# Optimization experiments

Hardware: AMD Instinct MI355X
Metric: run time of the kernel (lower is better)

The kernel has to match this reference:

```python
import jax, jax.numpy as jnp
import numpy as np

B, R, N, K, E = 128, 500, 500, 10, 128
H1 = 5 * E  # UnvisitedMLP hidden = embedding_dim * 5


def setup_inputs() -> dict:
    key = jax.random.key(0)
    ks = jax.random.split(key, 8)
    current = jax.random.randint(ks[0], (B, R), 0, N)
    distance = jax.random.uniform(ks[1], (B, N, N), dtype=jnp.float32)
    # unvisited cities, exercising the padding-index path in search_unvisited.
    visited = jax.random.uniform(ks[2], (B, R, N)) < 0.97
    masked = jnp.where(visited, -jnp.inf, 0.0).astype(jnp.float32)
    encoded_nodes = jax.random.normal(ks[3], (B, N, E), dtype=jnp.float32)
    w1 = jax.random.normal(ks[4], (H1, K * E), dtype=jnp.float32) * (1.0 / np.sqrt(K * E))
    b1 = jnp.zeros((H1,), dtype=jnp.float32)
    w2 = jax.random.normal(ks[5], (E, H1), dtype=jnp.float32) * (1.0 / np.sqrt(H1))
    b2 = jnp.zeros((E,), dtype=jnp.float32)
    return {"current": current, "distance": distance, "masked": masked,
            "encoded_nodes": encoded_nodes, "w1": w1, "b1": b1, "w2": w2, "b2": b2}


def _search_unvisited(current, distance, masked, k_near):
    # distance_filtered[b, r, :] = distance[b, current[b, r], :]  -> [B, R, N]
    b_idx = jnp.arange(current.shape[0])[:, None]
    distance_filtered = distance[b_idx, current, :]
    mask_unvisited = masked != -jnp.inf
    distance_masked = jnp.where(mask_unvisited, distance_filtered, jnp.inf)
    # k smallest == top-k of negated distances
    neg_vals, k_idx = jax.lax.top_k(-distance_masked, k_near)  # [B, R, K]
    is_inf = neg_vals == -jnp.inf  # entries that were +inf (no unvisited left)
    n_cities = distance.shape[1]
    return jnp.where(is_inf, n_cities, k_idx)  # padding index = problem_size


def _gather_pad0(encoded_nodes, idx):
    # pad encoded_nodes with a zero row at index N, then gather  -> [B, R, K, E]
    padded = jnp.concatenate(
        [encoded_nodes, jnp.zeros_like(encoded_nodes[:, :1, :])], axis=1)
    b_idx = jnp.arange(encoded_nodes.shape[0])[:, None, None]
    return padded[b_idx, idx, :]


def _pad_avg(a):
    # replace all-zero (padding) rows along K with the mean of non-zero rows
    is_zero = a.sum(axis=-1) == 0  # [B, R, K]
    nz_count = jnp.clip((~is_zero).sum(axis=-1).astype(jnp.float32), 1e-9)
    mean_vec = a.sum(axis=2) / nz_count[..., None]  # [B, R, E]
    return jnp.where(is_zero[..., None], mean_vec[:, :, None, :], a)


def reference(current, distance, masked, encoded_nodes, w1, b1, w2, b2):
    k_near = K
    idx = _search_unvisited(current, distance, masked, k_near)  # [B, R, K]
    emb = _gather_pad0(encoded_nodes, idx)                      # [B, R, K, E]
    emb = _pad_avg(emb)
    h = emb.reshape(emb.shape[0], emb.shape[1], k_near * emb.shape[-1])  # [B, R, K*E]
    h = jax.nn.relu(jnp.einsum('brf,hf->brh', h, w1) + b1)
    out = jnp.einsum('brh,eh->bre', h, w2) + b2  # [B, R, E]
    return out
```

## Files before the change

kernel.cpp:

```cpp
#include <hip/hip_runtime.h>
#include <cstdint>
#include <cstddef>

#define Bn   128
#define Rn   500
#define Nn   500
#define Kn   10
#define En   128
#define H1n  640
#define KEn  1280
#define Mn   (Bn * Rn)

typedef short s16x8 __attribute__((ext_vector_type(8)));
typedef float f32x4 __attribute__((ext_vector_type(4)));

__device__ __forceinline__ unsigned short f2bf(float x) {
    union { float f; unsigned int u; } v; v.f = x;
    unsigned int r = v.u + 0x7fffu + ((v.u >> 16) & 1u);
    return (unsigned short)(r >> 16);
}
__device__ __forceinline__ float bf2f(unsigned short u) {
    union { unsigned int u; float f; } v; v.u = ((unsigned int)u) << 16;
    return v.f;
}
__device__ __forceinline__ void gl2lds16(const void* g, void* l) {
    __builtin_amdgcn_global_load_lds(
        (const __attribute__((address_space(1))) unsigned int*)g,
        (__attribute__((address_space(3))) unsigned int*)l, 16, 0, 0);
}
__device__ __forceinline__ void drain_all() {
    asm volatile("s_waitcnt vmcnt(0) lgkmcnt(0)" ::: "memory");
}

__global__ void convw_kernel(const float* __restrict__ enc, const float* __restrict__ w1,
                             const float* __restrict__ w2,
                             unsigned short* __restrict__ encb, unsigned short* __restrict__ w1b,
                             unsigned short* __restrict__ w2b) {
    int i = blockIdx.x * 256 + threadIdx.x;
    if (i < (Bn * Nn * En) / 4) {
        float4 v = ((const float4*)enc)[i];
        ushort4 o; o.x = f2bf(v.x); o.y = f2bf(v.y); o.z = f2bf(v.z); o.w = f2bf(v.w);
        ((ushort4*)encb)[i] = o;
    }
    if (i < (H1n * KEn) / 4) {
        float4 v = ((const float4*)w1)[i];
        ushort4 o; o.x = f2bf(v.x); o.y = f2bf(v.y); o.z = f2bf(v.z); o.w = f2bf(v.w);
        ((ushort4*)w1b)[i] = o;
    }
    if (i < (En * H1n) / 4) {
        float4 v = ((const float4*)w2)[i];
        ushort4 o; o.x = f2bf(v.x); o.y = f2bf(v.y); o.z = f2bf(v.z); o.w = f2bf(v.w);
        ((ushort4*)w2b)[i] = o;
    }
}

__global__ __launch_bounds__(256) void select_kernel(const int* __restrict__ current,
                            const float* __restrict__ distance,
                            const float* __restrict__ masked,
                            const unsigned short* __restrict__ encb,
                            int* __restrict__ idx_out,
                            unsigned short* __restrict__ meanbb) {
    const int row  = blockIdx.x * 4 + (threadIdx.x >> 6);
    const int lane = threadIdx.x & 63;
    const int b    = row / Rn;
    const int cur  = current[row];
    const unsigned int* drow = (const unsigned int*)(distance + ((size_t)b * Nn + cur) * Nn);
    const unsigned int* mrow = (const unsigned int*)(masked + (size_t)row * Nn);

    unsigned long long key[8];
#pragma unroll
    for (int i = 0; i < 8; ++i) {
        int nn = lane + 64 * i;
        unsigned int fb = 0x7F800000u;
        if (nn < Nn) {
            unsigned int m = mrow[nn];
            unsigned int d = drow[nn];
            fb = (m == 0xFF800000u) ? 0x7F800000u : d;
        }
        key[i] = ((unsigned long long)fb << 32) | (unsigned int)nn;
    }

    int ids[Kn];
    int myid = Nn;
#pragma unroll
    for (int it = 0; it < Kn; ++it) {
        unsigned long long bk = key[0];
#pragma unroll
        for (int i = 1; i < 8; ++i) bk = (key[i] < bk) ? key[i] : bk;
#pragma unroll
        for (int off = 1; off < 64; off <<= 1) {
            unsigned long long ok = __shfl_xor(bk, off);
            bk = (ok < bk) ? ok : bk;
        }
        const int wid = ((bk >> 32) == 0x7F800000u) ? Nn : (int)(bk & 0xffffffffu);
        ids[it] = wid;
        if (lane == it) myid = wid;
#pragma unroll
        for (int i = 0; i < 8; ++i)
            if (key[i] == bk) key[i] = 0x7F800000FFFFFFFFull;
    }
    if (lane < Kn) idx_out[row * Kn + lane] = myid;

    const unsigned int* encu = (const unsigned int*)(encb + (size_t)b * Nn * En);
    float s0 = 0.f, s1 = 0.f; int cnt = 0;
#pragma unroll
    for (int k = 0; k < Kn; ++k) {
        const int id = ids[k];
        if (id < Nn) {
            unsigned int u = encu[id * (En / 2) + lane];
            s0 += bf2f((unsigned short)(u & 0xffffu));
            s1 += bf2f((unsigned short)(u >> 16));
            cnt++;
        }
    }
    float m0 = 0.f, m1 = 0.f;
    if (cnt > 0) { m0 = s0 / (float)cnt; m1 = s1 / (float)cnt; }
    unsigned int packed = (unsigned int)f2bf(m0) | ((unsigned int)f2bf(m1) << 16);
    ((unsigned int*)meanbb)[(size_t)row * (En / 2) + lane] = packed;
}

__global__ __launch_bounds__(256, 4) void gemm1_kernel(
        const unsigned short* __restrict__ encb, const unsigned short* __restrict__ meanbb,
        const int* __restrict__ idxb, const unsigned short* __restrict__ w1b,
        const float* __restrict__ b1, unsigned short* __restrict__ hbuf) {
    __shared__ alignas(16) unsigned short As[2][128 * 32];
    __shared__ alignas(16) unsigned short Bs[2][128 * 32];
    __shared__ int idxs[128 * Kn];

    const int p = blockIdx.x;
    const int L = (p & 7) * 313 + (p >> 3);
    if (L >= (Mn / 128) * (H1n / 128)) return;
    const int row0 = (L / 5) * 128;
    const int h0   = (L % 5) * 128;

    const int t    = threadIdx.x;
    const int lane = t & 63;
    const int wave = t >> 6;
    const int ln15 = lane & 15;
    const int q4   = lane >> 4;
    const int wm   = wave & 1;
    const int wn   = wave >> 1;

    for (int i = t; i < 128 * Kn; i += 256) idxs[i] = idxb[row0 * Kn + i];

    const int rl   = lane >> 2;
    const int sc   = lane & 3;
    const int coff = (sc ^ (rl & 3)) * 8;

    int lrow[2];
    const unsigned short* encB[2];
    const unsigned short* meanR[2];
    const unsigned short* w1R[2];
#pragma unroll
    for (int s = 0; s < 2; ++s) {
        lrow[s] = wave * 32 + s * 16 + rl;
        const int gr = row0 + lrow[s];
        const int bb = gr / Rn;
        encB[s]  = encb + (size_t)bb * Nn * En;
        meanR[s] = meanbb + (size_t)gr * En + coff;
        w1R[s]   = w1b + (size_t)(h0 + lrow[s]) * KEn + coff;
    }

    f32x4 acc[4][4];
#pragma unroll
    for (int i = 0; i < 4; ++i)
#pragma unroll
        for (int j = 0; j < 4; ++j)
            acc[i][j] = (f32x4){0.f, 0.f, 0.f, 0.f};

    auto issue = [&](int itk, int pb) {
        const int j   = itk >> 2;
        const int e0  = (itk & 3) * 32;
        const int kk0 = itk * 32;
#pragma unroll
        for (int s = 0; s < 2; ++s) {
            const int id = idxs[lrow[s] * Kn + j];
            const unsigned short* srcA = (id < Nn)
                ? (encB[s] + (size_t)id * En + e0 + coff)
                : (meanR[s] + e0);
            gl2lds16(srcA, &As[pb][(wave * 32 + s * 16) * 32]);
            gl2lds16(w1R[s] + kk0, &Bs[pb][(wave * 32 + s * 16) * 32]);
        }
    };

    drain_all();
    __syncthreads();
    issue(0, 0);

    for (int itk = 0; itk < KEn / 32; ++itk) {
        const int cur = itk & 1;
        drain_all();
        __syncthreads();
        if (itk + 1 < KEn / 32) issue(itk + 1, cur ^ 1);
        s16x8 af[4], bf[4];
#pragma unroll
        for (int i = 0; i < 4; ++i) {
            const int r = wm * 64 + i * 16 + ln15;
            af[i] = *(const s16x8*)&As[cur][r * 32 + (q4 ^ (r & 3)) * 8];
        }
#pragma unroll
        for (int jj = 0; jj < 4; ++jj) {
            const int r = wn * 64 + jj * 16 + ln15;
            bf[jj] = *(const s16x8*)&Bs[cur][r * 32 + (q4 ^ (r & 3)) * 8];
        }
#pragma unroll
        for (int i = 0; i < 4; ++i)
#pragma unroll
            for (int jj = 0; jj < 4; ++jj)
                acc[i][jj] = __builtin_amdgcn_mfma_f32_16x16x32_bf16(af[i], bf[jj], acc[i][jj], 0, 0, 0);
    }

#pragma unroll
    for (int i = 0; i < 4; ++i) {
#pragma unroll
        for (int jj = 0; jj < 4; ++jj) {
            const int h = h0 + wn * 64 + jj * 16 + ln15;
            const float bias = b1[h];
#pragma unroll
            for (int rg = 0; rg < 4; ++rg) {
                const int m = wm * 64 + i * 16 + q4 * 4 + rg;
                float vv = acc[i][jj][rg] + bias;
                vv = fmaxf(vv, 0.f);
                hbuf[(size_t)(row0 + m) * H1n + h] = f2bf(vv);
            }
        }
    }
}

__global__ __launch_bounds__(256, 4) void gemm2_kernel(
        const unsigned short* __restrict__ hbuf, const unsigned short* __restrict__ w2b,
        const float* __restrict__ b2, float* __restrict__ out) {
    __shared__ alignas(16) unsigned short As[2][128 * 32];
    __shared__ alignas(16) unsigned short Bs[2][128 * 32];

    const int row0 = blockIdx.x * 128;
    const int t    = threadIdx.x;
    const int lane = t & 63;
    const int wave = t >> 6;
    const int ln15 = lane & 15;
    const int q4   = lane >> 4;
    const int wm   = wave & 1;
    const int wn   = wave >> 1;

    const int rl   = lane >> 2;
    const int sc   = lane & 3;
    const int coff = (sc ^ (rl & 3)) * 8;

    const unsigned short* hrow[2];
    const unsigned short* w2row[2];
#pragma unroll
    for (int s = 0; s < 2; ++s) {
        const int lr = wave * 32 + s * 16 + rl;
        hrow[s]  = hbuf + (size_t)(row0 + lr) * H1n + coff;
        w2row[s] = w2b + (size_t)lr * H1n + coff;
    }

    f32x4 acc[4][4];
#pragma unroll
    for (int i = 0; i < 4; ++i)
#pragma unroll
        for (int j = 0; j < 4; ++j)
            acc[i][j] = (f32x4){0.f, 0.f, 0.f, 0.f};

    auto issue = [&](int itk, int pb) {
        const int kk0 = itk * 32;
#pragma unroll
        for (int s = 0; s < 2; ++s) {
            gl2lds16(hrow[s] + kk0, &As[pb][(wave * 32 + s * 16) * 32]);
            gl2lds16(w2row[s] + kk0, &Bs[pb][(wave * 32 + s * 16) * 32]);
        }
    };

    issue(0, 0);

    for (int itk = 0; itk < H1n / 32; ++itk) {
        const int cur = itk & 1;
        drain_all();
        __syncthreads();
        if (itk + 1 < H1n / 32) issue(itk + 1, cur ^ 1);
        s16x8 af[4], bf[4];
#pragma unroll
        for (int i = 0; i < 4; ++i) {
            const int r = wm * 64 + i * 16 + ln15;
            af[i] = *(const s16x8*)&As[cur][r * 32 + (q4 ^ (r & 3)) * 8];
        }
#pragma unroll
        for (int jj = 0; jj < 4; ++jj) {
            const int r = wn * 64 + jj * 16 + ln15;
            bf[jj] = *(const s16x8*)&Bs[cur][r * 32 + (q4 ^ (r & 3)) * 8];
        }
#pragma unroll
        for (int i = 0; i < 4; ++i)
#pragma unroll
            for (int jj = 0; jj < 4; ++jj)
                acc[i][jj] = __builtin_amdgcn_mfma_f32_16x16x32_bf16(af[i], bf[jj], acc[i][jj], 0, 0, 0);
    }

#pragma unroll
    for (int i = 0; i < 4; ++i) {
#pragma unroll
        for (int jj = 0; jj < 4; ++jj) {
            const int e = wn * 64 + jj * 16 + ln15;
            const float bias = b2[e];
#pragma unroll
            for (int rg = 0; rg < 4; ++rg) {
                const int m = wm * 64 + i * 16 + q4 * 4 + rg;
                out[(size_t)(row0 + m) * En + e] = acc[i][jj][rg] + bias;
            }
        }
    }
}

extern "C" void kernel_launch(void* const* d_in, const int* in_sizes, int n_in,
                              void* d_out, int out_size, void* d_ws, size_t ws_size,
                              hipStream_t stream) {
    const int*   current  = (const int*)d_in[0];
    const float* distance = (const float*)d_in[1];
    const float* masked   = (const float*)d_in[2];
    const float* encoded  = (const float*)d_in[3];
    const float* w1       = (const float*)d_in[4];
    const float* b1       = (const float*)d_in[5];
    const float* w2       = (const float*)d_in[6];
    const float* b2       = (const float*)d_in[7];
    float* out = (float*)d_out;

    char* ws = (char*)d_ws;
    const size_t OFF_IDX  = 0;
    const size_t OFF_ENCB = 2560000;
    const size_t OFF_MEAN = OFF_ENCB + 16384000;
    const size_t OFF_W1B  = OFF_MEAN + 16384000;
    const size_t OFF_W2B  = OFF_W1B + 1638400;
    const size_t OFF_H    = OFF_W2B + 163840;
    int*            idxb   = (int*)(ws + OFF_IDX);
    unsigned short* encb   = (unsigned short*)(ws + OFF_ENCB);
    unsigned short* meanbb = (unsigned short*)(ws + OFF_MEAN);
    unsigned short* w1b    = (unsigned short*)(ws + OFF_W1B);
    unsigned short* w2b    = (unsigned short*)(ws + OFF_W2B);
    unsigned short* hbuf   = (unsigned short*)(ws + OFF_H);

    convw_kernel<<<(Bn * Nn * En / 4 + 255) / 256, 256, 0, stream>>>(encoded, w1, w2, encb, w1b, w2b);
    select_kernel<<<Mn / 4, 256, 0, stream>>>(current, distance, masked, encb, idxb, meanbb);
    gemm1_kernel<<<2504, 256, 0, stream>>>(encb, meanbb, idxb, w1b, b1, hbuf);
    gemm2_kernel<<<Mn / 128, 256, 0, stream>>>(hbuf, w2b, b2, out);
}
```

Before: 478.0 us.

## Triple-buffer LDS tiles in both GEMMs with partial vmcnt waits

```diff
diff --git a/kernel.cpp b/kernel.cpp
--- a/kernel.cpp
+++ b/kernel.cpp
@@ -30,6 +30,12 @@
 }
 __device__ __forceinline__ void drain_all() {
     asm volatile("s_waitcnt vmcnt(0) lgkmcnt(0)" ::: "memory");
+}
+#define WAITV(n) asm volatile("s_waitcnt vmcnt(" #n ")" ::: "memory")
+__device__ __forceinline__ void pipe_barrier() {
+    __builtin_amdgcn_s_barrier();
+    asm volatile("" ::: "memory");
+    __builtin_amdgcn_sched_barrier(0);
 }
 
 __global__ void convw_kernel(const float* __restrict__ enc, const float* __restrict__ w1,
@@ -123,8 +129,8 @@
         const unsigned short* __restrict__ encb, const unsigned short* __restrict__ meanbb,
         const int* __restrict__ idxb, const unsigned short* __restrict__ w1b,
         const float* __restrict__ b1, unsigned short* __restrict__ hbuf) {
-    __shared__ alignas(16) unsigned short As[2][128 * 32];
-    __shared__ alignas(16) unsigned short Bs[2][128 * 32];
+    __shared__ alignas(16) unsigned short As[3][128 * 32];
+    __shared__ alignas(16) unsigned short Bs[3][128 * 32];
     __shared__ int idxs[128 * Kn];
 
     const int p = blockIdx.x;
@@ -183,15 +189,19 @@
         }
     };
 
-    drain_all();
     __syncthreads();
     issue(0, 0);
-
+    issue(1, 1);
+
+    int cur = 0, nxt = 2;
     for (int itk = 0; itk < KEn / 32; ++itk) {
-        const int cur = itk & 1;
-        drain_all();
-        __syncthreads();
-        if (itk + 1 < KEn / 32) issue(itk + 1, cur ^ 1);
+        WAITV(4);
+        pipe_barrier();
+        {
+            int pre = itk + 2;
+            if (pre > KEn / 32 - 1) pre = KEn / 32 - 1;
+            issue(pre, nxt);
+        }
         s16x8 af[4], bf[4];
 #pragma unroll
         for (int i = 0; i < 4; ++i) {
@@ -208,7 +218,10 @@
 #pragma unroll
             for (int jj = 0; jj < 4; ++jj)
                 acc[i][jj] = __builtin_amdgcn_mfma_f32_16x16x32_bf16(af[i], bf[jj], acc[i][jj], 0, 0, 0);
-    }
+        cur = (cur == 2) ? 0 : cur + 1;
+        nxt = (nxt == 2) ? 0 : nxt + 1;
+    }
+    drain_all();
 
 #pragma unroll
     for (int i = 0; i < 4; ++i) {
@@ -230,8 +243,8 @@
 __global__ __launch_bounds__(256, 4) void gemm2_kernel(
         const unsigned short* __restrict__ hbuf, const unsigned short* __restrict__ w2b,
         const float* __restrict__ b2, float* __restrict__ out) {
-    __shared__ alignas(16) unsigned short As[2][128 * 32];
-    __shared__ alignas(16) unsigned short Bs[2][128 * 32];
+    __shared__ alignas(16) unsigned short As[3][128 * 32];
+    __shared__ alignas(16) unsigned short Bs[3][128 * 32];
 
     const int row0 = blockIdx.x * 128;
     const int t    = threadIdx.x;
@@ -272,12 +285,17 @@
     };
 
     issue(0, 0);
-
+    issue(1, 1);
+
+    int cur = 0, nxt = 2;
     for (int itk = 0; itk < H1n / 32; ++itk) {
-        const int cur = itk & 1;
-        drain_all();
-        __syncthreads();
-        if (itk + 1 < H1n / 32) issue(itk + 1, cur ^ 1);
+        WAITV(4);
+        pipe_barrier();
+        {
+            int pre = itk + 2;
+            if (pre > H1n / 32 - 1) pre = H1n / 32 - 1;
+            issue(pre, nxt);
+        }
         s16x8 af[4], bf[4];
 #pragma unroll
         for (int i = 0; i < 4; ++i) {
@@ -294,7 +312,10 @@
 #pragma unroll
             for (int jj = 0; jj < 4; ++jj)
                 acc[i][jj] = __builtin_amdgcn_mfma_f32_16x16x32_bf16(af[i], bf[jj], acc[i][jj], 0, 0, 0);
-    }
+        cur = (cur == 2) ? 0 : cur + 1;
+        nxt = (nxt == 2) ? 0 : nxt + 1;
+    }
+    drain_all();
 
 #pragma unroll
     for (int i = 0; i < 4; ++i) {
```

Measured after the change: 526.9 us. 10.2% more time.

## Restructure gemm1 into 256x128 tiles with triple-buffered K=64 LDS pipeline

Applied to the files above, without the earlier changes.

```diff
diff --git a/kernel.cpp b/kernel.cpp
--- a/kernel.cpp
+++ b/kernel.cpp
@@ -30,6 +30,11 @@
 }
 __device__ __forceinline__ void drain_all() {
     asm volatile("s_waitcnt vmcnt(0) lgkmcnt(0)" ::: "memory");
+}
+#define WAITV(n) asm volatile("s_waitcnt vmcnt(" #n ")" ::: "memory")
+__device__ __forceinline__ void pipe_barrier() {
+    __builtin_amdgcn_s_barrier();
+    asm volatile("" ::: "memory");
 }
 
 __global__ void convw_kernel(const float* __restrict__ enc, const float* __restrict__ w1,
@@ -119,47 +124,55 @@
     ((unsigned int*)meanbb)[(size_t)row * (En / 2) + lane] = packed;
 }
 
-__global__ __launch_bounds__(256, 4) void gemm1_kernel(
+__global__ __launch_bounds__(512, 2) void gemm1_kernel(
         const unsigned short* __restrict__ encb, const unsigned short* __restrict__ meanbb,
         const int* __restrict__ idxb, const unsigned short* __restrict__ w1b,
         const float* __restrict__ b1, unsigned short* __restrict__ hbuf) {
-    __shared__ alignas(16) unsigned short As[2][128 * 32];
-    __shared__ alignas(16) unsigned short Bs[2][128 * 32];
-    __shared__ int idxs[128 * Kn];
-
-    const int p = blockIdx.x;
-    const int L = (p & 7) * 313 + (p >> 3);
-    if (L >= (Mn / 128) * (H1n / 128)) return;
-    const int row0 = (L / 5) * 128;
-    const int h0   = (L % 5) * 128;
+    extern __shared__ unsigned short lds[];
+    unsigned short* const As = lds;
+    unsigned short* const Bs = lds + 3 * 256 * 64;
+
+    const int p  = blockIdx.x;
+    const int x  = p & 7;
+    const int rk = p >> 3;
+    const int w  = (x < 2 ? x * 157 : 314 + (x - 2) * 156) + rk;
+    const int row0 = (w / 5) * 256;
+    const int h0   = (w % 5) * 128;
 
     const int t    = threadIdx.x;
     const int lane = t & 63;
     const int wave = t >> 6;
     const int ln15 = lane & 15;
     const int q4   = lane >> 4;
-    const int wm   = wave & 1;
-    const int wn   = wave >> 1;
-
-    for (int i = t; i < 128 * Kn; i += 256) idxs[i] = idxb[row0 * Kn + i];
-
-    const int rl   = lane >> 2;
-    const int sc   = lane & 3;
-    const int coff = (sc ^ (rl & 3)) * 8;
-
-    int lrow[2];
-    const unsigned short* encB[2];
-    const unsigned short* meanR[2];
-    const unsigned short* w1R[2];
-#pragma unroll
-    for (int s = 0; s < 2; ++s) {
-        lrow[s] = wave * 32 + s * 16 + rl;
-        const int gr = row0 + lrow[s];
-        const int bb = gr / Rn;
-        encB[s]  = encb + (size_t)bb * Nn * En;
-        meanR[s] = meanbb + (size_t)gr * En + coff;
-        w1R[s]   = w1b + (size_t)(h0 + lrow[s]) * KEn + coff;
-    }
+    const int wm4  = wave & 3;
+    const int wn   = wave >> 2;
+
+    const int rl8 = lane >> 3;
+    const int sc8 = lane & 7;
+    const int cof = (sc8 ^ rl8) * 8;
+
+    const unsigned short* encBp[4];
+    const unsigned short* meanRp[4];
+    int grA[4];
+#pragma unroll
+    for (int s = 0; s < 4; ++s) {
+        const int gr = row0 + s * 64 + wave * 8 + rl8;
+        grA[s]    = gr;
+        encBp[s]  = encb + (size_t)(gr / Rn) * Nn * En;
+        meanRp[s] = meanbb + (size_t)gr * En + cof;
+    }
+    const unsigned short* w1Rp[2];
+#pragma unroll
+    for (int s = 0; s < 2; ++s)
+        w1Rp[s] = w1b + (size_t)(h0 + s * 64 + wave * 8 + rl8) * KEn + cof;
+
+    int idr[4][Kn];
+#pragma unroll
+    for (int s = 0; s < 4; ++s)
+#pragma unroll
+        for (int j = 0; j < Kn; ++j)
+            idr[s][j] = idxb[grA[s] * Kn + j];
+    WAITV(0);
 
     f32x4 acc[4][4];
 #pragma unroll
@@ -168,47 +181,102 @@
         for (int j = 0; j < 4; ++j)
             acc[i][j] = (f32x4){0.f, 0.f, 0.f, 0.f};
 
-    auto issue = [&](int itk, int pb) {
-        const int j   = itk >> 2;
-        const int e0  = (itk & 3) * 32;
-        const int kk0 = itk * 32;
-#pragma unroll
-        for (int s = 0; s < 2; ++s) {
-            const int id = idxs[lrow[s] * Kn + j];
-            const unsigned short* srcA = (id < Nn)
-                ? (encB[s] + (size_t)id * En + e0 + coff)
-                : (meanR[s] + e0);
-            gl2lds16(srcA, &As[pb][(wave * 32 + s * 16) * 32]);
-            gl2lds16(w1R[s] + kk0, &Bs[pb][(wave * 32 + s * 16) * 32]);
-        }
+    auto stA = [&](int s, int j, int e0, int b) {
+        const int id = idr[s][j];
+        const unsigned short* src = (id < Nn)
+            ? (encBp[s] + (size_t)id * En + e0 + cof)
+            : (meanRp[s] + e0);
+        gl2lds16(src, As + (size_t)b * (256 * 64) + (s * 64 + wave * 8) * 64);
     };
-
-    drain_all();
-    __syncthreads();
-    issue(0, 0);
-
-    for (int itk = 0; itk < KEn / 32; ++itk) {
-        const int cur = itk & 1;
-        drain_all();
-        __syncthreads();
-        if (itk + 1 < KEn / 32) issue(itk + 1, cur ^ 1);
-        s16x8 af[4], bf[4];
-#pragma unroll
-        for (int i = 0; i < 4; ++i) {
-            const int r = wm * 64 + i * 16 + ln15;
-            af[i] = *(const s16x8*)&As[cur][r * 32 + (q4 ^ (r & 3)) * 8];
-        }
-#pragma unroll
-        for (int jj = 0; jj < 4; ++jj) {
-            const int r = wn * 64 + jj * 16 + ln15;
-            bf[jj] = *(const s16x8*)&Bs[cur][r * 32 + (q4 ^ (r & 3)) * 8];
-        }
-#pragma unroll
-        for (int i = 0; i < 4; ++i)
-#pragma unroll
-            for (int jj = 0; jj < 4; ++jj)
-                acc[i][jj] = __builtin_amdgcn_mfma_f32_16x16x32_bf16(af[i], bf[jj], acc[i][jj], 0, 0, 0);
-    }
+    auto stB = [&](int s, int kt, int b) {
+        gl2lds16(w1Rp[s] + kt * 64, Bs + (size_t)b * (128 * 64) + (s * 64 + wave * 8) * 64);
+    };
+    auto bundle0 = [&](int kt, int b) {
+        const int j = kt >> 1, e0 = (kt & 1) * 64;
+        stA(0, j, e0, b); stA(1, j, e0, b); stB(0, kt, b);
+    };
+    auto bundle1 = [&](int kt, int b) {
+        const int j = kt >> 1, e0 = (kt & 1) * 64;
+        stA(2, j, e0, b); stA(3, j, e0, b); stB(1, kt, b);
+    };
+
+    bundle0(0, 0); bundle1(0, 0);
+    bundle0(1, 1); bundle1(1, 1);
+    WAITV(6);
+    pipe_barrier();
+
+    const int rA = wm4 * 64 + ln15;
+    const int rB = wn  * 64 + ln15;
+    const int s7 = ln15 & 7;
+    const int sl0 = (q4 ^ s7) * 8;
+    const int sl1 = ((4 + q4) ^ s7) * 8;
+
+#define MFMA16(a, bvec, c) c = __builtin_amdgcn_mfma_f32_16x16x32_bf16(a, bvec, c, 0, 0, 0)
+
+#pragma unroll
+    for (int kt = 0; kt < 20; ++kt) {
+        const int cb = kt % 3;
+        const unsigned short* Ab = As + cb * (256 * 64);
+        const unsigned short* Bb = Bs + cb * (128 * 64);
+        s16x8 af0, af1, af2, af3, bq0, bq1;
+
+        af0 = *(const s16x8*)(Ab + (rA +  0) * 64 + sl0);
+        af1 = *(const s16x8*)(Ab + (rA + 16) * 64 + sl0);
+        af2 = *(const s16x8*)(Ab + (rA + 32) * 64 + sl0);
+        af3 = *(const s16x8*)(Ab + (rA + 48) * 64 + sl0);
+        bq0 = *(const s16x8*)(Bb + (rB +  0) * 64 + sl0);
+        bq1 = *(const s16x8*)(Bb + (rB + 16) * 64 + sl0);
+        if (kt + 2 < 20) bundle0(kt + 2, (kt + 2) % 3);
+        pipe_barrier();
+        __builtin_amdgcn_s_setprio(1);
+        MFMA16(af0, bq0, acc[0][0]); MFMA16(af1, bq0, acc[1][0]);
+        MFMA16(af2, bq0, acc[2][0]); MFMA16(af3, bq0, acc[3][0]);
+        MFMA16(af0, bq1, acc[0][1]); MFMA16(af1, bq1, acc[1][1]);
+        MFMA16(af2, bq1, acc[2][1]); MFMA16(af3, bq1, acc[3][1]);
+        __builtin_amdgcn_s_setprio(0);
+        pipe_barrier();
+
+        bq0 = *(const s16x8*)(Bb + (rB + 32) * 64 + sl0);
+        bq1 = *(const s16x8*)(Bb + (rB + 48) * 64 + sl0);
+        pipe_barrier();
+        __builtin_amdgcn_s_setprio(1);
+        MFMA16(af0, bq0, acc[0][2]); MFMA16(af1, bq0, acc[1][2]);
+        MFMA16(af2, bq0, acc[2][2]); MFMA16(af3, bq0, acc[3][2]);
+        MFMA16(af0, bq1, acc[0][3]); MFMA16(af1, bq1, acc[1][3]);
+        MFMA16(af2, bq1, acc[2][3]); MFMA16(af3, bq1, acc[3][3]);
+        __builtin_amdgcn_s_setprio(0);
+        pipe_barrier();
+
+        af0 = *(const s16x8*)(Ab + (rA +  0) * 64 + sl1);
+        af1 = *(const s16x8*)(Ab + (rA + 16) * 64 + sl1);
+        af2 = *(const s16x8*)(Ab + (rA + 32) * 64 + sl1);
+        af3 = *(const s16x8*)(Ab + (rA + 48) * 64 + sl1);
+        bq0 = *(const s16x8*)(Bb + (rB +  0) * 64 + sl1);
+        bq1 = *(const s16x8*)(Bb + (rB + 16) * 64 + sl1);
+        if (kt + 2 < 20) bundle1(kt + 2, (kt + 2) % 3);
+        pipe_barrier();
+        __builtin_amdgcn_s_setprio(1);
+        MFMA16(af0, bq0, acc[0][0]); MFMA16(af1, bq0, acc[1][0]);
+        MFMA16(af2, bq0, acc[2][0]); MFMA16(af3, bq0, acc[3][0]);
+        MFMA16(af0, bq1, acc[0][1]); MFMA16(af1, bq1, acc[1][1]);
+        MFMA16(af2, bq1, acc[2][1]); MFMA16(af3, bq1, acc[3][1]);
+        __builtin_amdgcn_s_setprio(0);
+        pipe_barrier();
+
+        bq0 = *(const s16x8*)(Bb + (rB + 32) * 64 + sl1);
+        bq1 = *(const s16x8*)(Bb + (rB + 48) * 64 + sl1);
+        pipe_barrier();
+        __builtin_amdgcn_s_setprio(1);
+        MFMA16(af0, bq0, acc[0][2]); MFMA16(af1, bq0, acc[1][2]);
+        MFMA16(af2, bq0, acc[2][2]); MFMA16(af3, bq0, acc[3][2]);
+        MFMA16(af0, bq1, acc[0][3]); MFMA16(af1, bq1, acc[1][3]);
+        MFMA16(af2, bq1, acc[2][3]); MFMA16(af3, bq1, acc[3][3]);
+        __builtin_amdgcn_s_setprio(0);
+        if (kt + 2 < 20)      { WAITV(6); }
+        else if (kt + 1 < 20) { WAITV(0); }
+        pipe_barrier();
+    }
+#undef MFMA16
 
 #pragma unroll
     for (int i = 0; i < 4; ++i) {
@@ -218,7 +286,7 @@
             const float bias = b1[h];
 #pragma unroll
             for (int rg = 0; rg < 4; ++rg) {
-                const int m = wm * 64 + i * 16 + q4 * 4 + rg;
+                const int m = wm4 * 64 + i * 16 + q4 * 4 + rg;
                 float vv = acc[i][jj][rg] + bias;
                 vv = fmaxf(vv, 0.f);
                 hbuf[(size_t)(row0 + m) * H1n + h] = f2bf(vv);
@@ -338,8 +406,15 @@
     unsigned short* w2b    = (unsigned short*)(ws + OFF_W2B);
     unsigned short* hbuf   = (unsigned short*)(ws + OFF_H);
 
+    static bool s_attr = false;
+    if (!s_attr) {
+        hipFuncSetAttribute(reinterpret_cast<const void*>(gemm1_kernel),
+                            hipFuncAttributeMaxDynamicSharedMemorySize, 147456);
+        s_attr = true;
+    }
+
     convw_kernel<<<(Bn * Nn * En / 4 + 255) / 256, 256, 0, stream>>>(encoded, w1, w2, encb, w1b, w2b);
     select_kernel<<<Mn / 4, 256, 0, stream>>>(current, distance, masked, encb, idxb, meanbb);
-    gemm1_kernel<<<2504, 256, 0, stream>>>(encb, meanbb, idxb, w1b, b1, hbuf);
+    gemm1_kernel<<<1250, 512, 147456, stream>>>(encb, meanbb, idxb, w1b, b1, hbuf);
     gemm2_kernel<<<Mn / 128, 256, 0, stream>>>(hbuf, w2b, b2, out);
 }
```

Result: no change. 469.4 us (-1.8%).
